# Optimization experiments

Measured on AMD Instinct MI355X. Metric: run time of the kernel, lower is better.

## Reference

```python
import jax, jax.numpy as jnp
import numpy as np

N_WIRES = 3  # state vector of 2^3 = 8 amplitudes, kept as [B,2,2,2]


def _rx(t):
    c = jnp.cos(t / 2); s = jnp.sin(t / 2)
    return jnp.stack([jnp.stack([c + 0j, -1j * s], -1),
                      jnp.stack([-1j * s, c + 0j], -1)], -2).astype(jnp.complex64)


def _ry(t):
    c = jnp.cos(t / 2); s = jnp.sin(t / 2)
    return jnp.stack([jnp.stack([c, -s], -1),
                      jnp.stack([s, c], -1)], -2).astype(jnp.complex64)


def _rz(t):
    e = jnp.exp(-1j * t / 2).astype(jnp.complex64)
    z = jnp.zeros_like(e)
    return jnp.stack([jnp.stack([e, z], -1),
                      jnp.stack([z, jnp.conj(e)], -1)], -2)


def apply_1q(state, mat, wire):
    # state: [B,2,2,2]; mat: [2,2] (shared) or [B,2,2] (per-sample)
    s = jnp.moveaxis(state, 1 + wire, 1)
    sh = s.shape
    s = s.reshape(sh[0], 2, -1)
    m = jnp.broadcast_to(mat, (sh[0], 2, 2))
    s = jnp.einsum('bij,bjk->bik', m, s)
    return jnp.moveaxis(s.reshape(sh), 1, 1 + wire)


def apply_crx(state, t, ctrl, tgt):
    # controlled-RX: apply rx(t) to target subspace where control bit == 1
    mat = _rx(t)  # [2,2]
    s = jnp.moveaxis(state, (1 + ctrl, 1 + tgt), (1, 2))  # [B,2(ctrl),2(tgt),2]
    s1 = s[:, 1]                       # [B,2,2]
    sh = s1.shape
    s1 = jnp.einsum('ij,bjk->bik', mat, s1.reshape(sh[0], 2, -1)).reshape(sh)
    s = jnp.stack([s[:, 0], s1], 1)
    return jnp.moveaxis(s, (1, 2), (1 + ctrl, 1 + tgt))


def _quantum_forward(x, theta, W1, b1, W2, b2):
    B = x.shape[0]
    state = jnp.zeros((B, 2, 2, 2), jnp.complex64).at[:, 0, 0, 0].set(1.0)
    # GeneralEncoder: rx(x0)@w0, ry(x1)@w1, rz(x2)@w2
    state = apply_1q(state, _rx(x[:, 0]), 0)
    state = apply_1q(state, _ry(x[:, 1]), 1)
    state = apply_1q(state, _rz(x[:, 2]), 2)
    # RandomLayer(n_ops=8): fixed representative 8-op trainable sequence
    state = apply_1q(state, _rx(theta[0]), 0)
    state = apply_1q(state, _ry(theta[1]), 1)
    state = apply_1q(state, _rz(theta[2]), 2)
    state = apply_crx(state, theta[3], 0, 1)
    state = apply_1q(state, _ry(theta[4]), 2)
    state = apply_1q(state, _rx(theta[5]), 1)
    state = apply_crx(state, theta[6], 1, 2)
    state = apply_1q(state, _rz(theta[7]), 0)
    # measurement -> 8 basis-state probabilities (matches Linear(8,32) head)
    probs = (state.real ** 2 + state.imag ** 2).reshape(B, 8)
    h = jax.nn.relu(probs @ W1 + b1)
    return h @ W2 + b2


def setup_inputs() -> dict:
    key = jax.random.key(0)
    ks = jax.random.split(key, 6)
    B = 2_000_000
    x = jax.random.normal(ks[0], (B, 3), jnp.float32)
    theta = jax.random.normal(ks[1], (8,), jnp.float32)
    W1 = jax.random.normal(ks[2], (8, 32), jnp.float32) * 0.35   # ~1/sqrt(8)
    b1 = jnp.zeros((32,), jnp.float32)
    W2 = jax.random.normal(ks[3], (32, 2), jnp.float32) * 0.18   # ~1/sqrt(32)
    b2 = jnp.zeros((2,), jnp.float32)
    return {"x": x, "theta": theta, "W1": W1, "b1": b1, "W2": W2, "b2": b2}


def reference(x, theta, W1, b1, W2, b2):
    return _quantum_forward(x, theta, W1, b1, W2, b2)
```

## Files before the change

kernel.cpp:

```cpp
#include <hip/hip_runtime.h>


__global__ __launch_bounds__(64) void q_precompute(
    const float* __restrict__ theta,
    const float* __restrict__ W1,
    const float* __restrict__ b1,
    const float* __restrict__ W2,
    const float* __restrict__ b2,
    float* __restrict__ tab)
{
    __shared__ float Ure[8][8];
    __shared__ float Uim[8][8];
    const int t = threadIdx.x;

    if (t < 8) {
        float cr[8], ci[8];
        #pragma unroll
        for (int r = 0; r < 8; ++r) { cr[r] = (r == t) ? 1.f : 0.f; ci[r] = 0.f; }

        auto rxmix = [&](int a, int b, float c_, float s_) {
            float ar = cr[a], ai = ci[a], br = cr[b], bi = ci[b];
            cr[a] = c_*ar + s_*bi;   ci[a] = c_*ai - s_*br;
            cr[b] = s_*ai + c_*br;   ci[b] = -s_*ar + c_*bi;
        };
        auto rymix = [&](int a, int b, float c_, float s_) {
            float ar = cr[a], ai = ci[a], br = cr[b], bi = ci[b];
            cr[a] = c_*ar - s_*br;   ci[a] = c_*ai - s_*bi;
            cr[b] = s_*ar + c_*br;   ci[b] = s_*ai + c_*bi;
        };
        auto zmul = [&](int r, float u, float v) {
            float xr = cr[r], xi = ci[r];
            cr[r] = xr*u - xi*v;  ci[r] = xr*v + xi*u;
        };

        float c, s;
        __sincosf(theta[0]*0.5f, &s, &c);
        rxmix(0,4,c,s); rxmix(1,5,c,s); rxmix(2,6,c,s); rxmix(3,7,c,s);
        __sincosf(theta[1]*0.5f, &s, &c);
        rymix(0,2,c,s); rymix(1,3,c,s); rymix(4,6,c,s); rymix(5,7,c,s);
        __sincosf(theta[2]*0.5f, &s, &c);
        #pragma unroll
        for (int r = 0; r < 8; ++r) zmul(r, c, (r & 1) ? s : -s);
        __sincosf(theta[3]*0.5f, &s, &c);
        rxmix(4,6,c,s); rxmix(5,7,c,s);
        __sincosf(theta[4]*0.5f, &s, &c);
        rymix(0,1,c,s); rymix(2,3,c,s); rymix(4,5,c,s); rymix(6,7,c,s);
        __sincosf(theta[5]*0.5f, &s, &c);
        rxmix(0,2,c,s); rxmix(1,3,c,s); rxmix(4,6,c,s); rxmix(5,7,c,s);
        __sincosf(theta[6]*0.5f, &s, &c);
        rxmix(2,3,c,s); rxmix(6,7,c,s);
        __sincosf(theta[7]*0.5f, &s, &c);
        #pragma unroll
        for (int r = 0; r < 8; ++r) zmul(r, c, (r < 4) ? -s : s);

        #pragma unroll
        for (int r = 0; r < 8; ++r) { Ure[r][t] = cr[r]; Uim[r][t] = ci[r]; }
    }
    __syncthreads();

    if (t < 32) {
        float Wre[8][4], Wim[8][4];
        #pragma unroll
        for (int j = 0; j < 8; ++j) {
            Wre[j][0] =  Ure[j][0]; Wim[j][0] =  Uim[j][0];
            Wre[j][1] =  Ure[j][2]; Wim[j][1] =  Uim[j][2];
            Wre[j][2] =  Uim[j][4]; Wim[j][2] = -Ure[j][4];
            Wre[j][3] =  Uim[j][6]; Wim[j][3] = -Ure[j][6];
        }
        float Q[4][4];
        #pragma unroll
        for (int m = 0; m < 4; ++m)
            #pragma unroll
            for (int n = 0; n < 4; ++n) Q[m][n] = 0.f;
        #pragma unroll
        for (int j = 0; j < 8; ++j) {
            float w = W1[j*32 + t];
            #pragma unroll
            for (int m = 0; m < 4; ++m)
                #pragma unroll
                for (int n = 0; n < 4; ++n)
                    Q[m][n] = fmaf(w, Wre[j][m]*Wre[j][n] + Wim[j][m]*Wim[j][n], Q[m][n]);
        }
        float R[3][3];
        R[0][0] = Q[0][0];
        R[0][1] = Q[0][1] + Q[1][0];
        R[0][2] = Q[1][1];
        R[1][0] = Q[0][2] + Q[2][0];
        R[1][1] = Q[0][3] + Q[1][2] + Q[2][1] + Q[3][0];
        R[1][2] = Q[1][3] + Q[3][1];
        R[2][0] = Q[2][2];
        R[2][1] = Q[2][3] + Q[3][2];
        R[2][2] = Q[3][3];
        float P[3][3];
        #pragma unroll
        for (int b = 0; b < 3; ++b) {
            P[0][b] = 0.5f*(R[0][b] + R[2][b]);
            P[1][b] = 0.5f*(R[0][b] - R[2][b]);
            P[2][b] = 0.5f*R[1][b];
        }
        float T[3][3];
        #pragma unroll
        for (int si = 0; si < 3; ++si) {
            T[si][0] = 0.5f*(P[si][0] + P[si][2]);
            T[si][1] = 0.5f*(P[si][0] - P[si][2]);
            T[si][2] = 0.5f*P[si][1];
        }
        float* row = tab + t*12;
        row[0] = T[0][1]; row[1] = T[0][2]; row[2] = T[1][0]; row[3] = T[2][0];
        row[4] = T[1][1]; row[5] = T[1][2]; row[6] = T[2][1]; row[7] = T[2][2];
        row[8] = b1[t] + T[0][0];
        row[9]  = W2[t*2+0];
        row[10] = W2[t*2+1];
        row[11] = 0.f;
    }
    if (t == 0) { tab[384] = b2[0]; tab[385] = b2[1]; tab[386] = 0.f; tab[387] = 0.f; }
}

#define INV_2PI 0.15915494309189535f

__global__ __launch_bounds__(256) void q_main(
    const float* __restrict__ x,
    const float* __restrict__ tab,
    float* __restrict__ out,
    int B)
{
    const int t    = blockIdx.x * 256 + threadIdx.x;
    const int base = t * 8;
    if (base >= B) return;

    const float b2a = tab[384], b2b = tab[385];

    if (base + 8 <= B) {
        float4 xa[6];
        const float4* X4 = (const float4*)x;
        #pragma unroll
        for (int i = 0; i < 6; ++i) xa[i] = X4[t*6 + i];

        const float* xf = (const float*)xa;
        float C0[8], S0[8], C1[8], S1[8], Pcc[8], Pcs[8], Psc[8], Pss[8];
        #pragma unroll
        for (int k = 0; k < 8; ++k) {
            float r0 = xf[3*k+0] * INV_2PI;
            float r1 = xf[3*k+1] * INV_2PI;
            S0[k] = __builtin_amdgcn_sinf(r0);
            C0[k] = __builtin_amdgcn_cosf(r0);
            S1[k] = __builtin_amdgcn_sinf(r1);
            C1[k] = __builtin_amdgcn_cosf(r1);
            Pcc[k] = C0[k]*C1[k]; Pcs[k] = C0[k]*S1[k];
            Psc[k] = S0[k]*C1[k]; Pss[k] = S0[k]*S1[k];
        }
        float acc0[8], acc1[8];
        #pragma unroll
        for (int k = 0; k < 8; ++k) { acc0[k] = b2a; acc1[k] = b2b; }

        const float4* T4 = (const float4*)tab;
        #pragma unroll 2
        for (int l = 0; l < 32; ++l) {
            float4 cA = T4[l*3+0];
            float4 cB = T4[l*3+1];
            float4 cC = T4[l*3+2];
            #pragma unroll
            for (int k = 0; k < 8; ++k) {
                float h = cC.x;
                h = fmaf(cA.x, C1[k],  h);
                h = fmaf(cA.y, S1[k],  h);
                h = fmaf(cA.z, C0[k],  h);
                h = fmaf(cA.w, S0[k],  h);
                h = fmaf(cB.x, Pcc[k], h);
                h = fmaf(cB.y, Pcs[k], h);
                h = fmaf(cB.z, Psc[k], h);
                h = fmaf(cB.w, Pss[k], h);
                h = fmaxf(h, 0.f);
                acc0[k] = fmaf(h, cC.y, acc0[k]);
                acc1[k] = fmaf(h, cC.z, acc1[k]);
            }
        }
        float4* O4 = (float4*)out;
        #pragma unroll
        for (int k = 0; k < 4; ++k)
            O4[t*4+k] = make_float4(acc0[2*k], acc1[2*k], acc0[2*k+1], acc1[2*k+1]);
    } else {
        for (int e = base; e < B; ++e) {
            float s0, c0, s1, c1;
            float r0 = x[e*3+0] * INV_2PI;
            float r1 = x[e*3+1] * INV_2PI;
            s0 = __builtin_amdgcn_sinf(r0); c0 = __builtin_amdgcn_cosf(r0);
            s1 = __builtin_amdgcn_sinf(r1); c1 = __builtin_amdgcn_cosf(r1);
            float pcc = c0*c1, pcs = c0*s1, psc = s0*c1, pss = s0*s1;
            float A0 = b2a, A1 = b2b;
            for (int l = 0; l < 32; ++l) {
                const float* row = tab + l*12;
                float h = row[8];
                h = fmaf(row[0], c1,  h);
                h = fmaf(row[1], s1,  h);
                h = fmaf(row[2], c0,  h);
                h = fmaf(row[3], s0,  h);
                h = fmaf(row[4], pcc, h);
                h = fmaf(row[5], pcs, h);
                h = fmaf(row[6], psc, h);
                h = fmaf(row[7], pss, h);
                h = fmaxf(h, 0.f);
                A0 = fmaf(h, row[9],  A0);
                A1 = fmaf(h, row[10], A1);
            }
            out[e*2+0] = A0;
            out[e*2+1] = A1;
        }
    }
}

extern "C" void kernel_launch(void* const* d_in, const int* in_sizes, int n_in,
                              void* d_out, int out_size, void* d_ws, size_t ws_size,
                              hipStream_t stream) {
    const float* x     = (const float*)d_in[0];
    const float* theta = (const float*)d_in[1];
    const float* W1    = (const float*)d_in[2];
    const float* b1    = (const float*)d_in[3];
    const float* W2    = (const float*)d_in[4];
    const float* b2    = (const float*)d_in[5];
    float* out = (float*)d_out;
    float* tab = (float*)d_ws;

    const int B = in_sizes[0] / 3;

    q_precompute<<<1, 64, 0, stream>>>(theta, W1, b1, W2, b2, tab);

    const int nT = (B + 7) / 8;
    const int blocks = (nT + 255) / 256;
    q_main<<<blocks, 256, 0, stream>>>(x, tab, out, B);
}
```

Before: 101.7 us.

## Use packed f32x2 FMAs and strided 4-elements-per-thread mapping in main kernel

Rewrites the main kernel so each thread processes 4 elements spaced by the block width instead of 8 consecutive ones, giving coalesced per-element loads/stores and twice as many threads. The hidden-layer dot products are expressed with 2-wide vector FMAs so the compiler can emit packed FP32 FMA instructions, halving the instruction count of the dominant ALU loop. Risk is extra register moves for broadcasting table scalars and less work per thread to amortize the table loads.

```diff
diff --git a/kernel.cpp b/kernel.cpp
--- a/kernel.cpp
+++ b/kernel.cpp
@@ -1,5 +1,14 @@
 #include <hip/hip_runtime.h>
 
+
+typedef float f32x2 __attribute__((ext_vector_type(2)));
+
+static __device__ __forceinline__ f32x2 pk_fma(f32x2 a, f32x2 b, f32x2 c) {
+    return __builtin_elementwise_fma(a, b, c);
+}
+static __device__ __forceinline__ f32x2 splat2(float v) {
+    f32x2 r; r.x = v; r.y = v; return r;
+}
 
 __global__ __launch_bounds__(64) void q_precompute(
     const float* __restrict__ theta,
@@ -124,84 +133,97 @@
     float* __restrict__ out,
     int B)
 {
-    const int t    = blockIdx.x * 256 + threadIdx.x;
-    const int base = t * 8;
-    if (base >= B) return;
+    const int lid = threadIdx.x;
+    const int bb  = blockIdx.x * 1024;
+    const int e0  = bb + lid;
 
     const float b2a = tab[384], b2b = tab[385];
-
-    if (base + 8 <= B) {
-        float4 xa[6];
-        const float4* X4 = (const float4*)x;
-        #pragma unroll
-        for (int i = 0; i < 6; ++i) xa[i] = X4[t*6 + i];
-
-        const float* xf = (const float*)xa;
-        float C0[8], S0[8], C1[8], S1[8], Pcc[8], Pcs[8], Psc[8], Pss[8];
-        #pragma unroll
-        for (int k = 0; k < 8; ++k) {
-            float r0 = xf[3*k+0] * INV_2PI;
-            float r1 = xf[3*k+1] * INV_2PI;
-            S0[k] = __builtin_amdgcn_sinf(r0);
-            C0[k] = __builtin_amdgcn_cosf(r0);
-            S1[k] = __builtin_amdgcn_sinf(r1);
-            C1[k] = __builtin_amdgcn_cosf(r1);
-            Pcc[k] = C0[k]*C1[k]; Pcs[k] = C0[k]*S1[k];
-            Psc[k] = S0[k]*C1[k]; Pss[k] = S0[k]*S1[k];
-        }
-        float acc0[8], acc1[8];
-        #pragma unroll
-        for (int k = 0; k < 8; ++k) { acc0[k] = b2a; acc1[k] = b2b; }
-
-        const float4* T4 = (const float4*)tab;
+    const float4* T4 = (const float4*)tab;
+
+    if (bb + 1024 <= B) {
+        float xs0[4], xs1[4];
+        #pragma unroll
+        for (int k = 0; k < 4; ++k) {
+            const int e = e0 + k*256;
+            xs0[k] = x[e*3 + 0];
+            xs1[k] = x[e*3 + 1];
+        }
+
+        f32x2 c0v[2], s0v[2], c1v[2], s1v[2], pcc[2], pcs[2], psc[2], pss[2];
+        #pragma unroll
+        for (int g = 0; g < 2; ++g) {
+            #pragma unroll
+            for (int j = 0; j < 2; ++j) {
+                const int k = 2*g + j;
+                const float r0 = xs0[k] * INV_2PI;
+                const float r1 = xs1[k] * INV_2PI;
+                s0v[g][j] = __builtin_amdgcn_sinf(r0);
+                c0v[g][j] = __builtin_amdgcn_cosf(r0);
+                s1v[g][j] = __builtin_amdgcn_sinf(r1);
+                c1v[g][j] = __builtin_amdgcn_cosf(r1);
+            }
+            pcc[g] = c0v[g]*c1v[g]; pcs[g] = c0v[g]*s1v[g];
+            psc[g] = s0v[g]*c1v[g]; pss[g] = s0v[g]*s1v[g];
+        }
+
+        f32x2 a0v[2], a1v[2];
+        #pragma unroll
+        for (int g = 0; g < 2; ++g) { a0v[g] = splat2(b2a); a1v[g] = splat2(b2b); }
+
         #pragma unroll 2
         for (int l = 0; l < 32; ++l) {
-            float4 cA = T4[l*3+0];
-            float4 cB = T4[l*3+1];
-            float4 cC = T4[l*3+2];
-            #pragma unroll
-            for (int k = 0; k < 8; ++k) {
-                float h = cC.x;
-                h = fmaf(cA.x, C1[k],  h);
-                h = fmaf(cA.y, S1[k],  h);
-                h = fmaf(cA.z, C0[k],  h);
-                h = fmaf(cA.w, S0[k],  h);
-                h = fmaf(cB.x, Pcc[k], h);
-                h = fmaf(cB.y, Pcs[k], h);
-                h = fmaf(cB.z, Psc[k], h);
-                h = fmaf(cB.w, Pss[k], h);
-                h = fmaxf(h, 0.f);
-                acc0[k] = fmaf(h, cC.y, acc0[k]);
-                acc1[k] = fmaf(h, cC.z, acc1[k]);
+            const float4 cA = T4[l*3+0];
+            const float4 cB = T4[l*3+1];
+            const float4 cC = T4[l*3+2];
+            #pragma unroll
+            for (int g = 0; g < 2; ++g) {
+                f32x2 h = pk_fma(splat2(cA.x), c1v[g], splat2(cC.x));
+                h = pk_fma(splat2(cA.y), s1v[g], h);
+                h = pk_fma(splat2(cA.z), c0v[g], h);
+                h = pk_fma(splat2(cA.w), s0v[g], h);
+                h = pk_fma(splat2(cB.x), pcc[g], h);
+                h = pk_fma(splat2(cB.y), pcs[g], h);
+                h = pk_fma(splat2(cB.z), psc[g], h);
+                h = pk_fma(splat2(cB.w), pss[g], h);
+                h = __builtin_elementwise_max(h, splat2(0.f));
+                a0v[g] = pk_fma(h, splat2(cC.y), a0v[g]);
+                a1v[g] = pk_fma(h, splat2(cC.z), a1v[g]);
             }
         }
-        float4* O4 = (float4*)out;
-        #pragma unroll
-        for (int k = 0; k < 4; ++k)
-            O4[t*4+k] = make_float4(acc0[2*k], acc1[2*k], acc0[2*k+1], acc1[2*k+1]);
+
+        f32x2* O2 = (f32x2*)out;
+        #pragma unroll
+        for (int k = 0; k < 4; ++k) {
+            const int e = e0 + k*256;
+            f32x2 o; o.x = a0v[k>>1][k&1]; o.y = a1v[k>>1][k&1];
+            O2[e] = o;
+        }
     } else {
-        for (int e = base; e < B; ++e) {
-            float s0, c0, s1, c1;
-            float r0 = x[e*3+0] * INV_2PI;
-            float r1 = x[e*3+1] * INV_2PI;
-            s0 = __builtin_amdgcn_sinf(r0); c0 = __builtin_amdgcn_cosf(r0);
-            s1 = __builtin_amdgcn_sinf(r1); c1 = __builtin_amdgcn_cosf(r1);
-            float pcc = c0*c1, pcs = c0*s1, psc = s0*c1, pss = s0*s1;
+        for (int k = 0; k < 4; ++k) {
+            const int e = e0 + k*256;
+            if (e >= B) continue;
+            const float r0 = x[e*3+0] * INV_2PI;
+            const float r1 = x[e*3+1] * INV_2PI;
+            const float s0 = __builtin_amdgcn_sinf(r0), c0 = __builtin_amdgcn_cosf(r0);
+            const float s1 = __builtin_amdgcn_sinf(r1), c1 = __builtin_amdgcn_cosf(r1);
+            const float pc = c0*c1, ps = c0*s1, sc = s0*c1, ss = s0*s1;
             float A0 = b2a, A1 = b2b;
             for (int l = 0; l < 32; ++l) {
-                const float* row = tab + l*12;
-                float h = row[8];
-                h = fmaf(row[0], c1,  h);
-                h = fmaf(row[1], s1,  h);
-                h = fmaf(row[2], c0,  h);
-                h = fmaf(row[3], s0,  h);
-                h = fmaf(row[4], pcc, h);
-                h = fmaf(row[5], pcs, h);
-                h = fmaf(row[6], psc, h);
-                h = fmaf(row[7], pss, h);
+                const float4 cA = T4[l*3+0];
+                const float4 cB = T4[l*3+1];
+                const float4 cC = T4[l*3+2];
+                float h = cC.x;
+                h = fmaf(cA.x, c1, h);
+                h = fmaf(cA.y, s1, h);
+                h = fmaf(cA.z, c0, h);
+                h = fmaf(cA.w, s0, h);
+                h = fmaf(cB.x, pc, h);
+                h = fmaf(cB.y, ps, h);
+                h = fmaf(cB.z, sc, h);
+                h = fmaf(cB.w, ss, h);
                 h = fmaxf(h, 0.f);
-                A0 = fmaf(h, row[9],  A0);
-                A1 = fmaf(h, row[10], A1);
+                A0 = fmaf(h, cC.y, A0);
+                A1 = fmaf(h, cC.z, A1);
             }
             out[e*2+0] = A0;
             out[e*2+1] = A1;
@@ -225,7 +247,6 @@
 
     q_precompute<<<1, 64, 0, stream>>>(theta, W1, b1, W2, b2, tab);
 
-    const int nT = (B + 7) / 8;
-    const int blocks = (nT + 255) / 256;
+    const int blocks = (B + 1023) / 1024;
     q_main<<<blocks, 256, 0, stream>>>(x, tab, out, B);
 }
```

Result: faster. 97.79 us (-3.9%).
